# Optimization experiments

Hardware: AMD Instinct MI355X
Metric: run time of the kernel (lower is better)

Reference implementation:

```python
import jax, jax.numpy as jnp
import numpy as np

H = 8  # num_heads


def _ln(x, g, b):
    mu = x.mean(-1, keepdims=True)
    var = ((x - mu) ** 2).mean(-1, keepdims=True)
    return (x - mu) * jax.lax.rsqrt(var + 1e-5) * g + b


def setup_inputs() -> dict:
    key = jax.random.key(0)
    ks = jax.random.split(key, 24)
    B, N, V, E, D, R, L = 8, 512, 50000, 300, 256, 100, 4
    dh = D // H
    s = 0.02
    inp = {}
    inp['token_ids'] = jax.random.randint(ks[0], (B, N), 0, V, dtype=jnp.int32)
    inp['relations'] = jax.random.randint(ks[1], (B, N, N), 0, R, dtype=jnp.int32)
    m = jax.random.bernoulli(ks[2], 0.9, (B, N, N))
    eye = jnp.eye(N, dtype=bool)[None]
    inp['relations_mask'] = jnp.logical_or(m, eye)  # keep diagonal valid so every row attends somewhere
    inp['embed'] = jax.random.normal(ks[3], (V, E), jnp.float32) * s
    inp['W_in'] = jax.random.normal(ks[4], (E, D), jnp.float32) * s
    inp['b_in'] = jnp.zeros((D,), jnp.float32)
    inp['Wq'] = jax.random.normal(ks[5], (L, D, D), jnp.float32) * s
    inp['Wk'] = jax.random.normal(ks[6], (L, D, D), jnp.float32) * s
    inp['Wv'] = jax.random.normal(ks[7], (L, D, D), jnp.float32) * s
    inp['Wo'] = jax.random.normal(ks[8], (L, D, D), jnp.float32) * s
    inp['ln1_g'] = jnp.ones((L, D), jnp.float32)
    inp['ln1_b'] = jnp.zeros((L, D), jnp.float32)
    inp['ln2_g'] = jnp.ones((L, D), jnp.float32)
    inp['ln2_b'] = jnp.zeros((L, D), jnp.float32)
    inp['W1'] = jax.random.normal(ks[9], (L, D, 4 * D), jnp.float32) * s
    inp['b1'] = jnp.zeros((L, 4 * D), jnp.float32)
    inp['W2'] = jax.random.normal(ks[10], (L, 4 * D, D), jnp.float32) * s
    inp['b2'] = jnp.zeros((L, D), jnp.float32)
    inp['rel_k_emb'] = jax.random.normal(ks[11], (R, dh), jnp.float32) * s
    inp['rel_v_emb'] = jax.random.normal(ks[12], (R, dh), jnp.float32) * s
    inp['W_out'] = jax.random.normal(ks[13], (D, D), jnp.float32) * s
    inp['b_out'] = jnp.zeros((D,), jnp.float32)
    return inp


def reference(token_ids, relations, relations_mask, embed, W_in, b_in, Wq, Wk, Wv, Wo,
              ln1_g, ln1_b, ln2_g, ln2_b, W1, b1, W2, b2, rel_k_emb, rel_v_emb, W_out, b_out):
    # Input layer: embedding lookup + projection to gnn hidden size.
    x = embed[token_ids]                          # [B,N,E]
    x = jax.nn.relu(x @ W_in + b_in)              # [B,N,D]
    B, N, D = x.shape
    dh = D // H
    # Shared relation embeddings (share_layers=True, share_heads=True): gathered once.
    rk = rel_k_emb[relations]                     # [B,N,N,dh]
    rv = rel_v_emb[relations]                     # [B,N,N,dh]
    neg = jnp.asarray(-1e9, x.dtype)
    scale = jnp.asarray(1.0 / np.sqrt(dh), x.dtype)
    L = Wq.shape[0]
    for l in range(L):  # fixed small layer count
        q = (x @ Wq[l]).reshape(B, N, H, dh).transpose(0, 2, 1, 3)
        k = (x @ Wk[l]).reshape(B, N, H, dh).transpose(0, 2, 1, 3)
        v = (x @ Wv[l]).reshape(B, N, H, dh).transpose(0, 2, 1, 3)
        # Relation-aware scores: q.k + q.r_k (RAT-SQL)
        scores = (jnp.einsum('bhnd,bhmd->bhnm', q, k)
                  + jnp.einsum('bhnd,bnmd->bhnm', q, rk)) * scale
        scores = jnp.where(relations_mask[:, None], scores, neg)
        a = jax.nn.softmax(scores, axis=-1)       # [B,H,N,N]
        z = (jnp.einsum('bhnm,bhmd->bhnd', a, v)
             + jnp.einsum('bhnm,bnmd->bhnd', a, rv))
        z = z.transpose(0, 2, 1, 3).reshape(B, N, D) @ Wo[l]
        x = _ln(x + z, ln1_g[l], ln1_b[l])
        f = jax.nn.relu(x @ W1[l] + b1[l]) @ W2[l] + b2[l]
        x = _ln(x + f, ln2_g[l], ln2_b[l])
    # Output layer projection
    return x @ W_out + b_out
```

## Files before the change

kernel.cpp:

```cpp
#include <hip/hip_runtime.h>
#include <hip/hip_bf16.h>

#define NTOK 4096
#define NN   512

typedef __attribute__((ext_vector_type(8))) short bf16x8;
typedef __attribute__((ext_vector_type(4))) short bf16x4;
typedef __attribute__((ext_vector_type(4))) float f32x4;

__device__ __forceinline__ float bf16_to_f(unsigned short u) {
    unsigned int x = ((unsigned int)u) << 16;
    return __builtin_bit_cast(float, x);
}
__device__ __forceinline__ unsigned short f_to_bf16(float f) {
    unsigned int b = __builtin_bit_cast(unsigned int, f);
    return (unsigned short)((b + 0x7fff + ((b >> 16) & 1)) >> 16);
}
__device__ __forceinline__ bf16x8 pack8(float4 a, float4 b) {
    bf16x8 v;
    v[0]=(short)f_to_bf16(a.x); v[1]=(short)f_to_bf16(a.y);
    v[2]=(short)f_to_bf16(a.z); v[3]=(short)f_to_bf16(a.w);
    v[4]=(short)f_to_bf16(b.x); v[5]=(short)f_to_bf16(b.y);
    v[6]=(short)f_to_bf16(b.z); v[7]=(short)f_to_bf16(b.w);
    return v;
}

__global__ void detect_mask_kernel(const unsigned char* __restrict__ m, int* __restrict__ flag) {
    __shared__ int f;
    if (threadIdx.x == 0) f = 0;
    __syncthreads();
    int any = 0;
    for (int i = threadIdx.x; i < 4096; i += 256) {
        if ((i & 3) != 0 && m[i] != 0) any = 1;
    }
    if (any) atomicOr(&f, 1);
    __syncthreads();
    if (threadIdx.x == 0) *flag = f;
}

__global__ __launch_bounds__(256) void prep_rel16(
    const int* __restrict__ rel, const void* __restrict__ mask,
    const int* __restrict__ flag, short* __restrict__ rel16)
{
    const bool mbyte = (*flag != 0);
    const unsigned char* m8 = (const unsigned char*)mask;
    const int* m32 = (const int*)mask;
    const int i = (blockIdx.x * 256 + threadIdx.x) * 2;
    int2 rv = *(const int2*)(rel + i);
    int ok0, ok1;
    if (mbyte) { ok0 = m8[i]; ok1 = m8[i + 1]; }
    else       { ok0 = (m32[i] != 0); ok1 = (m32[i + 1] != 0); }
    short2 o;
    o.x = ok0 ? (short)rv.x : (short)-1;
    o.y = ok1 ? (short)rv.y : (short)-1;
    *(short2*)(rel16 + i) = o;
}

__global__ __launch_bounds__(256) void embed_proj_kernel(
    const int* __restrict__ tok, const float* __restrict__ embed,
    const float* __restrict__ W_in, const float* __restrict__ b_in,
    float* __restrict__ x)
{
    __shared__ float emb[8][304];
    __shared__ int tloc[8];
    const int t = threadIdx.x;
    const int r0 = blockIdx.x * 8;
    if (t < 8) tloc[t] = tok[r0 + t];
    __syncthreads();
    for (int i = t; i < 8 * 300; i += 256) {
        int r = i / 300, e = i - r * 300;
        emb[r][e] = embed[(size_t)tloc[r] * 300 + e];
    }
    __syncthreads();
    float acc[8] = {0.f,0.f,0.f,0.f,0.f,0.f,0.f,0.f};
    const int d = t;
    for (int e = 0; e < 300; ++e) {
        float w = W_in[e * 256 + d];
#pragma unroll
        for (int r = 0; r < 8; ++r) acc[r] += emb[r][e] * w;
    }
    const float bb = b_in[d];
#pragma unroll
    for (int r = 0; r < 8; ++r) {
        float o = acc[r] + bb;
        o = o > 0.f ? o : 0.f;
        x[(size_t)(r0 + r) * 256 + d] = o;
    }
}

__global__ __launch_bounds__(256) void gemm_mfma(
    const float* __restrict__ A,
    const float* __restrict__ W0, const float* __restrict__ W1p, const float* __restrict__ W2p,
    int ncPerW, const float* __restrict__ bias,
    float* __restrict__ C, int M, int K, int Nc, int relu)
{
    __shared__ unsigned short As[2][64][40];
    __shared__ unsigned short Bs[2][64][40];

    const int t = threadIdx.x;
    const int lane = t & 63, w = t >> 6;
    const int g = lane >> 4, li = lane & 15;
    const int r0 = blockIdx.y * 64, c0 = blockIdx.x * 64;

    const float* Wp = W0; int cW = c0;
    if (c0 >= 2 * ncPerW)      { Wp = W2p; cW = c0 - 2 * ncPerW; }
    else if (c0 >= ncPerW)     { Wp = W1p; cW = c0 - ncPerW; }

    f32x4 acc[4];
#pragma unroll
    for (int i = 0; i < 4; ++i) acc[i] = (f32x4){0.f, 0.f, 0.f, 0.f};

    const int arow = t >> 2, ad8 = (t & 3) * 8;
    const int bnn = t & 63, bk8 = (t >> 6) * 8;

    const float* ap0 = A + (size_t)(r0 + arow) * K + ad8;
    float4 a0 = *(const float4*)ap0;
    float4 a1 = *(const float4*)(ap0 + 4);
    float wv[8];
#pragma unroll
    for (int j = 0; j < 8; ++j)
        wv[j] = Wp[(size_t)(bk8 + j) * ncPerW + cW + bnn];

    const int nk = K >> 5;
    for (int ki = 0; ki < nk; ++ki) {
        const int cur = ki & 1;
        *(bf16x8*)&As[cur][arow][ad8] = pack8(a0, a1);
        {
            bf16x8 v;
#pragma unroll
            for (int j = 0; j < 8; ++j) v[j] = (short)f_to_bf16(wv[j]);
            *(bf16x8*)&Bs[cur][bnn][bk8] = v;
        }
        if (ki + 1 < nk) {
            const int k0 = (ki + 1) * 32;
            const float* ap = A + (size_t)(r0 + arow) * K + k0 + ad8;
            a0 = *(const float4*)ap;
            a1 = *(const float4*)(ap + 4);
#pragma unroll
            for (int j = 0; j < 8; ++j)
                wv[j] = Wp[(size_t)(k0 + bk8 + j) * ncPerW + cW + bnn];
        }
        __syncthreads();
        bf16x8 af = *(const bf16x8*)&As[cur][16 * w + li][g * 8];
#pragma unroll
        for (int sub = 0; sub < 4; ++sub) {
            bf16x8 bfr = *(const bf16x8*)&Bs[cur][16 * sub + li][g * 8];
            acc[sub] = __builtin_amdgcn_mfma_f32_16x16x32_bf16(af, bfr, acc[sub], 0, 0, 0);
        }
    }
#pragma unroll
    for (int sub = 0; sub < 4; ++sub) {
        int col = c0 + sub * 16 + li;
        float bv = bias ? bias[col] : 0.f;
#pragma unroll
        for (int r = 0; r < 4; ++r) {
            int row = r0 + 16 * w + g * 4 + r;
            float o = acc[sub][r] + bv;
            if (relu) o = fmaxf(o, 0.f);
            C[(size_t)row * Nc + col] = o;
        }
    }
}

__global__ __launch_bounds__(256) void attn_mfma(
    const float* __restrict__ qkv,
    const short* __restrict__ rel16,
    const float* __restrict__ relk_g,
    const float* __restrict__ relv_g,
    float* __restrict__ zout)
{
    const int p = blockIdx.x;
    const int cx = p & 7, kk = p >> 3;
    const int bc = cx * 8 + (kk >> 3);
    const int h  = kk & 7;
    const int b  = bc >> 3;
    const int n0 = (bc & 7) * 64;

    const int t = threadIdx.x;
    const int lane = t & 63, w = t >> 6;
    const int g = lane >> 4, li = lane & 15;
    const int qrow = 16 * w + g * 4;

    __shared__ float wrel[64][100];
    __shared__ unsigned short qrk[64][100];
    __shared__ union {
        unsigned short relk_s[100][40];
        unsigned short relvT[32][136];
        struct {
            unsigned short k_t[2][32][40];
            unsigned short v_t[2][32][40];
            unsigned short p_s[4][16][40];
        } mn;
    } u;

    for (int i = t; i < 6400; i += 256) ((float*)wrel)[i] = 0.f;
    for (int i = t; i < 400; i += 256) {
        int rr = i >> 2, d8 = (i & 3) * 8;
        const float* sp = relk_g + rr * 32 + d8;
        *(bf16x8*)&u.relk_s[rr][d8] = pack8(*(const float4*)sp, *(const float4*)(sp + 4));
    }
    const float scale = 0.17677669529663687f;
    bf16x8 qf;
    {
        const float* qp = qkv + (size_t)(b * NN + n0 + 16 * w + li) * 768 + h * 32 + g * 8;
        float4 q0 = *(const float4*)qp, q1 = *(const float4*)(qp + 4);
        q0.x *= scale; q0.y *= scale; q0.z *= scale; q0.w *= scale;
        q1.x *= scale; q1.y *= scale; q1.z *= scale; q1.w *= scale;
        qf = pack8(q0, q1);
    }
    __syncthreads();

#pragma unroll
    for (int rc = 0; rc < 7; ++rc) {
        bf16x8 bb = *(const bf16x8*)&u.relk_s[rc * 16 + li][g * 8];
        f32x4 s = __builtin_amdgcn_mfma_f32_16x16x32_bf16(qf, bb, (f32x4){0.f,0.f,0.f,0.f}, 0, 0, 0);
        int col = rc * 16 + li;
        if (col < 100) {
#pragma unroll
            for (int r = 0; r < 4; ++r)
                qrk[qrow + r][col] = f_to_bf16(s[r]);
        }
    }

    float smacc[4] = {0.f, 0.f, 0.f, 0.f};
    f32x4 zf[2];
    zf[0] = (f32x4){0.f,0.f,0.f,0.f};
    zf[1] = (f32x4){0.f,0.f,0.f,0.f};

    const short* relrow[4];
#pragma unroll
    for (int r = 0; r < 4; ++r)
        relrow[r] = rel16 + ((size_t)b * NN + n0 + qrow + r) * NN;

    const int krow = t >> 3, kd4 = (t & 7) * 4;
    const int vm = t & 31, vdg = t >> 5;
    const size_t kbase0 = (size_t)(b * NN) * 768 + 256 + h * 32;
    const size_t vbase0 = (size_t)(b * NN) * 768 + 512 + h * 32;

    float4 kreg = *(const float4*)(qkv + kbase0 + (size_t)krow * 768 + kd4);
    float4 vreg = *(const float4*)(qkv + vbase0 + (size_t)vm * 768 + vdg * 4);
    short rr[8], rn[8];
#pragma unroll
    for (int idx = 0; idx < 8; ++idx)
        rr[idx] = relrow[idx & 3][(idx >> 2) * 16 + li];

    __syncthreads();

    for (int mt = 0; mt < 16; ++mt) {
        const int cur = mt & 1;
        {
            bf16x4 kv;
            kv[0]=(short)f_to_bf16(kreg.x); kv[1]=(short)f_to_bf16(kreg.y);
            kv[2]=(short)f_to_bf16(kreg.z); kv[3]=(short)f_to_bf16(kreg.w);
            *(bf16x4*)&u.mn.k_t[cur][krow][kd4] = kv;
        }
        {
            u.mn.v_t[cur][vdg * 4 + 0][vm] = f_to_bf16(vreg.x);
            u.mn.v_t[cur][vdg * 4 + 1][vm] = f_to_bf16(vreg.y);
            u.mn.v_t[cur][vdg * 4 + 2][vm] = f_to_bf16(vreg.z);
            u.mn.v_t[cur][vdg * 4 + 3][vm] = f_to_bf16(vreg.w);
        }
        if (mt + 1 < 16) {
            const int m0n = (mt + 1) * 32;
            kreg = *(const float4*)(qkv + kbase0 + (size_t)(m0n + krow) * 768 + kd4);
            vreg = *(const float4*)(qkv + vbase0 + (size_t)(m0n + vm) * 768 + vdg * 4);
#pragma unroll
            for (int idx = 0; idx < 8; ++idx)
                rn[idx] = relrow[idx & 3][m0n + (idx >> 2) * 16 + li];
        }
        __syncthreads();

        bf16x8 kf0 = *(const bf16x8*)&u.mn.k_t[cur][li][g * 8];
        bf16x8 kf1 = *(const bf16x8*)&u.mn.k_t[cur][16 + li][g * 8];
        f32x4 s0 = __builtin_amdgcn_mfma_f32_16x16x32_bf16(qf, kf0, (f32x4){0.f,0.f,0.f,0.f}, 0, 0, 0);
        f32x4 s1 = __builtin_amdgcn_mfma_f32_16x16x32_bf16(qf, kf1, (f32x4){0.f,0.f,0.f,0.f}, 0, 0, 0);

        float pr[8];
#pragma unroll
        for (int idx = 0; idx < 8; ++idx) {
            const int r = idx & 3;
            const int rl = rr[idx];
            const int rla = rl < 0 ? 0 : rl;
            const float qadd = bf16_to_f(qrk[qrow + r][rla]);
            const float sv = ((idx >> 2) ? s1[r] : s0[r]) + qadd;
            float pv = 0.f;
            if (rl >= 0) {
                pv = __expf(fminf(sv, 50.f));
                atomicAdd(&wrel[qrow + r][rl], pv);
            }
            smacc[r] += pv;
            pr[idx] = pv;
        }
#pragma unroll
        for (int idx = 0; idx < 8; ++idx)
            u.mn.p_s[w][g * 4 + (idx & 3)][(idx >> 2) * 16 + li] = f_to_bf16(pr[idx]);

        asm volatile("s_waitcnt lgkmcnt(0)" ::: "memory");
        __builtin_amdgcn_sched_barrier(0);

        bf16x8 pa = *(const bf16x8*)&u.mn.p_s[w][li][g * 8];
#pragma unroll
        for (int dc = 0; dc < 2; ++dc) {
            bf16x8 vb = *(const bf16x8*)&u.mn.v_t[cur][dc * 16 + li][g * 8];
            zf[dc] = __builtin_amdgcn_mfma_f32_16x16x32_bf16(pa, vb, zf[dc], 0, 0, 0);
        }
#pragma unroll
        for (int idx = 0; idx < 8; ++idx) rr[idx] = rn[idx];
    }
    __syncthreads();

    for (int i = t; i < 32 * 36; i += 256) {
        int d = i / 36, c = 100 + (i - (i / 36) * 36);
        u.relvT[d][c] = 0;
    }
    for (int i = t; i < 400; i += 256) {
        int rr2 = i >> 2, d8 = (i & 3) * 8;
        const float* sp = relv_g + rr2 * 32 + d8;
        float4 s0 = *(const float4*)sp, s1 = *(const float4*)(sp + 4);
        u.relvT[d8 + 0][rr2] = f_to_bf16(s0.x);
        u.relvT[d8 + 1][rr2] = f_to_bf16(s0.y);
        u.relvT[d8 + 2][rr2] = f_to_bf16(s0.z);
        u.relvT[d8 + 3][rr2] = f_to_bf16(s0.w);
        u.relvT[d8 + 4][rr2] = f_to_bf16(s1.x);
        u.relvT[d8 + 5][rr2] = f_to_bf16(s1.y);
        u.relvT[d8 + 6][rr2] = f_to_bf16(s1.z);
        u.relvT[d8 + 7][rr2] = f_to_bf16(s1.w);
    }
    __syncthreads();

#pragma unroll
    for (int kc = 0; kc < 4; ++kc) {
        const int kbase = kc * 32 + g * 8;
        const float* wp = &wrel[16 * w + li][0];
        bf16x8 af;
#pragma unroll
        for (int j = 0; j < 8; ++j) {
            int idx = kbase + j;
            float val = (idx < 100) ? wp[idx] : 0.f;
            af[j] = (short)f_to_bf16(val);
        }
#pragma unroll
        for (int dc = 0; dc < 2; ++dc) {
            bf16x8 vb = *(const bf16x8*)&u.relvT[dc * 16 + li][kbase];
            zf[dc] = __builtin_amdgcn_mfma_f32_16x16x32_bf16(af, vb, zf[dc], 0, 0, 0);
        }
    }

#pragma unroll
    for (int r = 0; r < 4; ++r) {
        smacc[r] += __shfl_xor(smacc[r], 1, 64);
        smacc[r] += __shfl_xor(smacc[r], 2, 64);
        smacc[r] += __shfl_xor(smacc[r], 4, 64);
        smacc[r] += __shfl_xor(smacc[r], 8, 64);
    }
#pragma unroll
    for (int r = 0; r < 4; ++r) {
        float inv = 1.f / smacc[r];
        size_t ob = ((size_t)(b * NN + n0 + qrow + r)) * 256 + h * 32;
#pragma unroll
        for (int dc = 0; dc < 2; ++dc)
            zout[ob + dc * 16 + li] = zf[dc][r] * inv;
    }
}

__global__ __launch_bounds__(256) void ln_kernel(
    const float* __restrict__ xin, const float* __restrict__ y,
    const float* __restrict__ g, const float* __restrict__ bsh,
    float* __restrict__ xout)
{
    const int t = threadIdx.x;
    const int w = t >> 6, lane = t & 63;
    const size_t row = (size_t)blockIdx.x * 4 + w;
    const float4 xv = *(const float4*)(xin + row * 256 + lane * 4);
    const float4 yv = *(const float4*)(y + row * 256 + lane * 4);
    float4 sv;
    sv.x = xv.x + yv.x; sv.y = xv.y + yv.y; sv.z = xv.z + yv.z; sv.w = xv.w + yv.w;
    float sum = sv.x + sv.y + sv.z + sv.w;
    float sq  = sv.x * sv.x + sv.y * sv.y + sv.z * sv.z + sv.w * sv.w;
#pragma unroll
    for (int off = 1; off < 64; off <<= 1) {
        sum += __shfl_xor(sum, off, 64);
        sq  += __shfl_xor(sq, off, 64);
    }
    const float mu = sum * (1.f / 256.f);
    const float var = sq * (1.f / 256.f) - mu * mu;
    const float rs = rsqrtf(var + 1e-5f);
    const float4 gv = *(const float4*)(g + lane * 4);
    const float4 bv = *(const float4*)(bsh + lane * 4);
    float4 o;
    o.x = (sv.x - mu) * rs * gv.x + bv.x;
    o.y = (sv.y - mu) * rs * gv.y + bv.y;
    o.z = (sv.z - mu) * rs * gv.z + bv.z;
    o.w = (sv.w - mu) * rs * gv.w + bv.w;
    *(float4*)(xout + row * 256 + lane * 4) = o;
}

extern "C" void kernel_launch(void* const* d_in, const int* in_sizes, int n_in,
                              void* d_out, int out_size, void* d_ws, size_t ws_size,
                              hipStream_t stream)
{
    (void)in_sizes; (void)n_in; (void)out_size;
    const int*   tok   = (const int*)d_in[0];
    const int*   rel   = (const int*)d_in[1];
    const void*  mask  = d_in[2];
    const float* embed = (const float*)d_in[3];
    const float* W_in  = (const float*)d_in[4];
    const float* b_in  = (const float*)d_in[5];
    const float* Wq    = (const float*)d_in[6];
    const float* Wk    = (const float*)d_in[7];
    const float* Wv    = (const float*)d_in[8];
    const float* Wo    = (const float*)d_in[9];
    const float* ln1g  = (const float*)d_in[10];
    const float* ln1b  = (const float*)d_in[11];
    const float* ln2g  = (const float*)d_in[12];
    const float* ln2b  = (const float*)d_in[13];
    const float* W1    = (const float*)d_in[14];
    const float* b1    = (const float*)d_in[15];
    const float* W2    = (const float*)d_in[16];
    const float* b2    = (const float*)d_in[17];
    const float* relk  = (const float*)d_in[18];
    const float* relv  = (const float*)d_in[19];
    const float* Wout  = (const float*)d_in[20];
    const float* bout  = (const float*)d_in[21];
    float* out = (float*)d_out;

    float* ws  = (float*)d_ws;
    float* x   = ws;
    float* z   = ws + (1u << 20);
    float* zo  = ws + 2u * (1u << 20);
    float* qkv = ws + 3u * (1u << 20);
    float* hb  = ws + 6u * (1u << 20);

    const bool roomy = ws_size >= ((size_t)48 << 20);
    short* rel16 = roomy ? (short*)(ws + 10u * (1u << 20)) : (short*)hb;
    int*   flag  = (int*)(ws + (roomy ? 11u : 10u) * (1u << 20));

    detect_mask_kernel<<<1, 256, 0, stream>>>((const unsigned char*)mask, flag);
    if (roomy)
        prep_rel16<<<4096, 256, 0, stream>>>(rel, mask, flag, rel16);
    embed_proj_kernel<<<512, 256, 0, stream>>>(tok, embed, W_in, b_in, x);

    for (int l = 0; l < 4; ++l) {
        const float* wq = Wq + (size_t)l * 65536;
        const float* wk = Wk + (size_t)l * 65536;
        const float* wv = Wv + (size_t)l * 65536;
        const float* wo = Wo + (size_t)l * 65536;
        const float* w1 = W1 + (size_t)l * 262144;
        const float* w2 = W2 + (size_t)l * 262144;

        if (!roomy)
            prep_rel16<<<4096, 256, 0, stream>>>(rel, mask, flag, rel16);

        gemm_mfma<<<dim3(12, 64), 256, 0, stream>>>(x, wq, wk, wv, 256, nullptr,
                                                    qkv, NTOK, 256, 768, 0);
        attn_mfma<<<512, 256, 0, stream>>>(qkv, rel16, relk, relv, z);
        gemm_mfma<<<dim3(4, 64), 256, 0, stream>>>(z, wo, wo, wo, 256, nullptr,
                                                   zo, NTOK, 256, 256, 0);
        ln_kernel<<<1024, 256, 0, stream>>>(x, zo, ln1g + l * 256, ln1b + l * 256, x);
        gemm_mfma<<<dim3(16, 64), 256, 0, stream>>>(x, w1, w1, w1, 1024, b1 + l * 1024,
                                                    hb, NTOK, 256, 1024, 1);
        gemm_mfma<<<dim3(4, 64), 256, 0, stream>>>(hb, w2, w2, w2, 256, b2 + l * 256,
                                                   zo, NTOK, 1024, 256, 0);
        ln_kernel<<<1024, 256, 0, stream>>>(x, zo, ln2g + l * 256, ln2b + l * 256, x);
    }
    gemm_mfma<<<dim3(4, 64), 256, 0, stream>>>(x, Wout, Wout, Wout, 256, bout,
                                               out, NTOK, 256, 256, 0);
}
```

Baseline: 638.0 us.

## Split attention over key chunks with partial sums and a combine kernel

Splits each attention block's 512 keys into four 128-key slices, launching 2048 blocks instead of 512. Each block writes unnormalized partial outputs and partial softmax denominators, and a new combine kernel sums them and normalizes. K is now loaded straight into registers and packed to bf16 rather than staged through LDS, and loads are prefetched across an unrolled 4-step loop. The aim is to fill more CUs and hide latency, at the cost of an extra kernel launch, extra global traffic for the partials, and redoing the per-block qrk/relk setup four times.

```diff
diff --git a/kernel.cpp b/kernel.cpp
--- a/kernel.cpp
+++ b/kernel.cpp
@@ -162,19 +162,20 @@
     }
 }
 
-__global__ __launch_bounds__(256) void attn_mfma(
+__global__ __launch_bounds__(256, 3) void attn_mfma(
     const float* __restrict__ qkv,
     const short* __restrict__ rel16,
     const float* __restrict__ relk_g,
     const float* __restrict__ relv_g,
-    float* __restrict__ zout)
+    float* __restrict__ zpart,
+    float* __restrict__ smpart)
 {
     const int p = blockIdx.x;
     const int cx = p & 7, kk = p >> 3;
-    const int bc = cx * 8 + (kk >> 3);
+    const int sg = cx * 32 + (kk >> 3);
     const int h  = kk & 7;
-    const int b  = bc >> 3;
-    const int n0 = (bc & 7) * 64;
+    const int b = sg >> 5, chunk = (sg >> 2) & 7, ms = sg & 3;
+    const int n0 = chunk * 64, mbase = ms * 128;
 
     const int t = threadIdx.x;
     const int lane = t & 63, w = t >> 6;
@@ -187,7 +188,6 @@
         unsigned short relk_s[100][40];
         unsigned short relvT[32][136];
         struct {
-            unsigned short k_t[2][32][40];
             unsigned short v_t[2][32][40];
             unsigned short p_s[4][16][40];
         } mn;
@@ -208,6 +208,27 @@
         q1.x *= scale; q1.y *= scale; q1.z *= scale; q1.w *= scale;
         qf = pack8(q0, q1);
     }
+
+    const short* relrow[4];
+#pragma unroll
+    for (int r = 0; r < 4; ++r)
+        relrow[r] = rel16 + ((size_t)b * NN + n0 + qrow + r) * NN;
+    const int vm = t & 31, vdg = t >> 5;
+    const size_t kRB = (size_t)(b * NN) * 768 + 256 + h * 32 + g * 8;
+    const size_t vRB = (size_t)(b * NN) * 768 + 512 + h * 32 + vdg * 4;
+
+    float4 kld[4][4]; float4 vld[4]; short rld[4][8];
+    {
+        const int m0 = mbase;
+        kld[0][0] = *(const float4*)(qkv + kRB + (size_t)(m0 + li) * 768);
+        kld[0][1] = *(const float4*)(qkv + kRB + (size_t)(m0 + li) * 768 + 4);
+        kld[0][2] = *(const float4*)(qkv + kRB + (size_t)(m0 + 16 + li) * 768);
+        kld[0][3] = *(const float4*)(qkv + kRB + (size_t)(m0 + 16 + li) * 768 + 4);
+        vld[0]    = *(const float4*)(qkv + vRB + (size_t)(m0 + vm) * 768);
+#pragma unroll
+        for (int idx = 0; idx < 8; ++idx)
+            rld[0][idx] = relrow[idx & 3][m0 + (idx >> 2) * 16 + li];
+    }
     __syncthreads();
 
 #pragma unroll
@@ -221,65 +242,47 @@
                 qrk[qrow + r][col] = f_to_bf16(s[r]);
         }
     }
+    __syncthreads();
 
     float smacc[4] = {0.f, 0.f, 0.f, 0.f};
     f32x4 zf[2];
     zf[0] = (f32x4){0.f,0.f,0.f,0.f};
     zf[1] = (f32x4){0.f,0.f,0.f,0.f};
 
-    const short* relrow[4];
-#pragma unroll
-    for (int r = 0; r < 4; ++r)
-        relrow[r] = rel16 + ((size_t)b * NN + n0 + qrow + r) * NN;
-
-    const int krow = t >> 3, kd4 = (t & 7) * 4;
-    const int vm = t & 31, vdg = t >> 5;
-    const size_t kbase0 = (size_t)(b * NN) * 768 + 256 + h * 32;
-    const size_t vbase0 = (size_t)(b * NN) * 768 + 512 + h * 32;
-
-    float4 kreg = *(const float4*)(qkv + kbase0 + (size_t)krow * 768 + kd4);
-    float4 vreg = *(const float4*)(qkv + vbase0 + (size_t)vm * 768 + vdg * 4);
-    short rr[8], rn[8];
-#pragma unroll
-    for (int idx = 0; idx < 8; ++idx)
-        rr[idx] = relrow[idx & 3][(idx >> 2) * 16 + li];
-
-    __syncthreads();
-
-    for (int mt = 0; mt < 16; ++mt) {
-        const int cur = mt & 1;
+#pragma unroll
+    for (int tt = 0; tt < 4; ++tt) {
+        const int cur = tt & 1;
         {
-            bf16x4 kv;
-            kv[0]=(short)f_to_bf16(kreg.x); kv[1]=(short)f_to_bf16(kreg.y);
-            kv[2]=(short)f_to_bf16(kreg.z); kv[3]=(short)f_to_bf16(kreg.w);
-            *(bf16x4*)&u.mn.k_t[cur][krow][kd4] = kv;
-        }
-        {
-            u.mn.v_t[cur][vdg * 4 + 0][vm] = f_to_bf16(vreg.x);
-            u.mn.v_t[cur][vdg * 4 + 1][vm] = f_to_bf16(vreg.y);
-            u.mn.v_t[cur][vdg * 4 + 2][vm] = f_to_bf16(vreg.z);
-            u.mn.v_t[cur][vdg * 4 + 3][vm] = f_to_bf16(vreg.w);
-        }
-        if (mt + 1 < 16) {
-            const int m0n = (mt + 1) * 32;
-            kreg = *(const float4*)(qkv + kbase0 + (size_t)(m0n + krow) * 768 + kd4);
-            vreg = *(const float4*)(qkv + vbase0 + (size_t)(m0n + vm) * 768 + vdg * 4);
+            float4 vv = vld[tt];
+            u.mn.v_t[cur][vdg * 4 + 0][vm] = f_to_bf16(vv.x);
+            u.mn.v_t[cur][vdg * 4 + 1][vm] = f_to_bf16(vv.y);
+            u.mn.v_t[cur][vdg * 4 + 2][vm] = f_to_bf16(vv.z);
+            u.mn.v_t[cur][vdg * 4 + 3][vm] = f_to_bf16(vv.w);
+        }
+        __syncthreads();
+        bf16x8 kf0 = pack8(kld[tt][0], kld[tt][1]);
+        bf16x8 kf1 = pack8(kld[tt][2], kld[tt][3]);
+        short rcur[8];
+#pragma unroll
+        for (int idx = 0; idx < 8; ++idx) rcur[idx] = rld[tt][idx];
+        if (tt + 1 < 4) {
+            const int m0n = mbase + (tt + 1) * 32;
+            kld[tt+1][0] = *(const float4*)(qkv + kRB + (size_t)(m0n + li) * 768);
+            kld[tt+1][1] = *(const float4*)(qkv + kRB + (size_t)(m0n + li) * 768 + 4);
+            kld[tt+1][2] = *(const float4*)(qkv + kRB + (size_t)(m0n + 16 + li) * 768);
+            kld[tt+1][3] = *(const float4*)(qkv + kRB + (size_t)(m0n + 16 + li) * 768 + 4);
+            vld[tt+1]    = *(const float4*)(qkv + vRB + (size_t)(m0n + vm) * 768);
 #pragma unroll
             for (int idx = 0; idx < 8; ++idx)
-                rn[idx] = relrow[idx & 3][m0n + (idx >> 2) * 16 + li];
-        }
-        __syncthreads();
-
-        bf16x8 kf0 = *(const bf16x8*)&u.mn.k_t[cur][li][g * 8];
-        bf16x8 kf1 = *(const bf16x8*)&u.mn.k_t[cur][16 + li][g * 8];
+                rld[tt+1][idx] = relrow[idx & 3][m0n + (idx >> 2) * 16 + li];
+        }
         f32x4 s0 = __builtin_amdgcn_mfma_f32_16x16x32_bf16(qf, kf0, (f32x4){0.f,0.f,0.f,0.f}, 0, 0, 0);
         f32x4 s1 = __builtin_amdgcn_mfma_f32_16x16x32_bf16(qf, kf1, (f32x4){0.f,0.f,0.f,0.f}, 0, 0, 0);
-
         float pr[8];
 #pragma unroll
         for (int idx = 0; idx < 8; ++idx) {
             const int r = idx & 3;
-            const int rl = rr[idx];
+            const int rl = rcur[idx];
             const int rla = rl < 0 ? 0 : rl;
             const float qadd = bf16_to_f(qrk[qrow + r][rla]);
             const float sv = ((idx >> 2) ? s1[r] : s0[r]) + qadd;
@@ -297,15 +300,12 @@
 
         asm volatile("s_waitcnt lgkmcnt(0)" ::: "memory");
         __builtin_amdgcn_sched_barrier(0);
-
         bf16x8 pa = *(const bf16x8*)&u.mn.p_s[w][li][g * 8];
 #pragma unroll
         for (int dc = 0; dc < 2; ++dc) {
             bf16x8 vb = *(const bf16x8*)&u.mn.v_t[cur][dc * 16 + li][g * 8];
             zf[dc] = __builtin_amdgcn_mfma_f32_16x16x32_bf16(pa, vb, zf[dc], 0, 0, 0);
         }
-#pragma unroll
-        for (int idx = 0; idx < 8; ++idx) rr[idx] = rn[idx];
     }
     __syncthreads();
 
@@ -355,12 +355,35 @@
     }
 #pragma unroll
     for (int r = 0; r < 4; ++r) {
-        float inv = 1.f / smacc[r];
-        size_t ob = ((size_t)(b * NN + n0 + qrow + r)) * 256 + h * 32;
+        const int row = b * NN + n0 + qrow + r;
+        size_t ob = (size_t)ms * 1048576 + (size_t)row * 256 + h * 32;
 #pragma unroll
         for (int dc = 0; dc < 2; ++dc)
-            zout[ob + dc * 16 + li] = zf[dc][r] * inv;
-    }
+            zpart[ob + dc * 16 + li] = zf[dc][r];
+        if (li == 0)
+            smpart[(size_t)ms * 32768 + (size_t)row * 8 + h] = smacc[r];
+    }
+}
+
+__global__ __launch_bounds__(256) void combine_kernel(
+    const float* __restrict__ zpart, const float* __restrict__ smpart,
+    float* __restrict__ z)
+{
+    const int t = threadIdx.x;
+    const int wi = t >> 6, lane = t & 63;
+    const int row = blockIdx.x * 4 + wi;
+    const int h = lane >> 3;
+    float den = 0.f;
+    float4 acc = make_float4(0.f, 0.f, 0.f, 0.f);
+#pragma unroll
+    for (int s = 0; s < 4; ++s) {
+        den += smpart[(size_t)s * 32768 + (size_t)row * 8 + h];
+        float4 v = *(const float4*)(zpart + (size_t)s * 1048576 + (size_t)row * 256 + lane * 4);
+        acc.x += v.x; acc.y += v.y; acc.z += v.z; acc.w += v.w;
+    }
+    const float inv = 1.f / den;
+    acc.x *= inv; acc.y *= inv; acc.z *= inv; acc.w *= inv;
+    *(float4*)(z + (size_t)row * 256 + lane * 4) = acc;
 }
 
 __global__ __launch_bounds__(256) void ln_kernel(
@@ -431,9 +454,11 @@
     float* qkv = ws + 3u * (1u << 20);
     float* hb  = ws + 6u * (1u << 20);
 
-    const bool roomy = ws_size >= ((size_t)48 << 20);
-    short* rel16 = roomy ? (short*)(ws + 10u * (1u << 20)) : (short*)hb;
+    const bool roomy = ws_size >= ((size_t)45 << 20);
+    short* rel16 = roomy ? (short*)(ws + 10u * (1u << 20)) : (short*)z;
     int*   flag  = (int*)(ws + (roomy ? 11u : 10u) * (1u << 20));
+    float* zpart = hb;
+    float* smpart = zo;
 
     detect_mask_kernel<<<1, 256, 0, stream>>>((const unsigned char*)mask, flag);
     if (roomy)
@@ -453,7 +478,8 @@
 
         gemm_mfma<<<dim3(12, 64), 256, 0, stream>>>(x, wq, wk, wv, 256, nullptr,
                                                     qkv, NTOK, 256, 768, 0);
-        attn_mfma<<<512, 256, 0, stream>>>(qkv, rel16, relk, relv, z);
+        attn_mfma<<<2048, 256, 0, stream>>>(qkv, rel16, relk, relv, zpart, smpart);
+        combine_kernel<<<1024, 256, 0, stream>>>(zpart, smpart, z);
         gemm_mfma<<<dim3(4, 64), 256, 0, stream>>>(z, wo, wo, wo, 256, nullptr,
                                                    zo, NTOK, 256, 256, 0);
         ln_kernel<<<1024, 256, 0, stream>>>(x, zo, ln1g + l * 256, ln1b + l * 256, x);
```

After: 702.8 us. +10.2%, slower.
